# Optimization experiments

Hardware: AMD Instinct MI355X
Metric: run time of the kernel (lower is better)

The kernel has to match this reference:

```python
import jax, jax.numpy as jnp
import numpy as np

N, S, D_IN, D_OUT = 8192, 3, 32, 32


def setup_inputs() -> dict:
    key = jax.random.key(0)
    k1, k2, k3, k4 = jax.random.split(key, 4)
    x = jax.random.normal(k1, (N, D_IN), dtype=jnp.float32)
    adj = jax.random.normal(k2, (S, N, N), dtype=jnp.float32) * 0.01
    # Linear weights per support (W stored as [in, out]; torch Linear is x @ W.T + b,
    # here we store the already-transposed form so pre = x @ W[s] + b[s]).
    W = jax.random.normal(k3, (S, D_IN, D_OUT), dtype=jnp.float32) * (1.0 / np.sqrt(D_IN))
    b = jax.random.normal(k4, (S, D_OUT), dtype=jnp.float32) * 0.01
    return {"x": x, "adj": adj, "W": W, "b": b}


def reference(x, adj, W, b):
    # dropout p=0.0 -> identity
    # per-support linear: pre[s] = x @ W[s] + b[s]  -> [S, N, D_OUT]
    pre = jnp.einsum('ni,sio->sno', x, W) + b[:, None, :]
    # graph propagation + sum over supports: sum_s adj[s] @ pre[s] -> [N, D_OUT]
    out = jnp.einsum('smn,sno->mo', adj, pre)
    return jax.nn.relu(out)
```

## Files before the change

kernel.cpp:

```cpp
#include <hip/hip_runtime.h>
#include <stdint.h>
#include <stddef.h>

static constexpr int NN = 8192;
static constexpr int DD = 32;
static constexpr int SS = 3;

typedef __attribute__((ext_vector_type(8))) short short8;
typedef __attribute__((ext_vector_type(4))) float floatx4;

__device__ __forceinline__ unsigned short f2bf(float f) {
  unsigned int u = __float_as_uint(f);
  u += 0x7FFFu + ((u >> 16) & 1u);
  return (unsigned short)(u >> 16);
}

extern "C" __global__ void __launch_bounds__(256)
pre_kernel(const float* __restrict__ x, const float* __restrict__ W,
           const float* __restrict__ b, unsigned short* __restrict__ preT) {
  __shared__ float xs[256 * 33];
  __shared__ float Ws[DD * DD];
  __shared__ float bs[DD];
  const int t = threadIdx.x;
  const int s = blockIdx.y;
  const int kbase = blockIdx.x * 256;

  #pragma unroll
  for (int j = 0; j < 32; ++j) {
    int idx = j * 256 + t;
    xs[(idx >> 5) * 33 + (idx & 31)] = x[kbase * DD + idx];
  }
  #pragma unroll
  for (int j = 0; j < 4; ++j) Ws[j * 256 + t] = W[s * DD * DD + j * 256 + t];
  if (t < DD) bs[t] = b[s * DD + t];
  __syncthreads();

  float xr[32];
  #pragma unroll
  for (int i = 0; i < 32; ++i) xr[i] = xs[t * 33 + i];

  unsigned short* o = preT + (size_t)s * DD * NN + kbase + t;
  #pragma unroll
  for (int n = 0; n < DD; ++n) {
    float acc = bs[n];
    #pragma unroll
    for (int i = 0; i < 32; ++i) acc += xr[i] * Ws[i * DD + n];
    o[(size_t)n * NN] = f2bf(acc);
  }
}

extern "C" __global__ void __launch_bounds__(512)
prop_kernel(const float* __restrict__ adj, const unsigned short* __restrict__ preT,
            float* __restrict__ out) {
  const int tid  = threadIdx.x;
  const int wave = tid >> 6;
  const int lane = tid & 63;
  const int q = lane >> 4;
  const int c = lane & 15;
  const int m0 = blockIdx.x * 16;

  const float* abase = adj + (size_t)(m0 + c) * NN + q * 8;
  const unsigned short* bbase = preT + (size_t)c * NN + q * 8;

  floatx4 acc0 = {0.f, 0.f, 0.f, 0.f};
  floatx4 acc1 = {0.f, 0.f, 0.f, 0.f};

  #pragma unroll 2
  for (int it = 0; it < 96; ++it) {
    const int st = wave + (it << 3);
    const int s  = st >> 8;
    const int k0 = (st & 255) << 5;

    const float* ap = abase + (size_t)s * NN * NN + k0;
    floatx4 alo = *(const floatx4*)ap;
    floatx4 ahi = *(const floatx4*)(ap + 4);

    const unsigned short* bp = bbase + (size_t)s * DD * NN + k0;
    short8 b0 = *(const short8*)bp;
    short8 b1 = *(const short8*)(bp + (size_t)16 * NN);

    short8 a;
    a[0] = (short)f2bf(alo[0]); a[1] = (short)f2bf(alo[1]);
    a[2] = (short)f2bf(alo[2]); a[3] = (short)f2bf(alo[3]);
    a[4] = (short)f2bf(ahi[0]); a[5] = (short)f2bf(ahi[1]);
    a[6] = (short)f2bf(ahi[2]); a[7] = (short)f2bf(ahi[3]);

    acc0 = __builtin_amdgcn_mfma_f32_16x16x32_bf16(a, b0, acc0, 0, 0, 0);
    acc1 = __builtin_amdgcn_mfma_f32_16x16x32_bf16(a, b1, acc1, 0, 0, 0);
  }

  __shared__ float red[8 * 512];
  #pragma unroll
  for (int r = 0; r < 4; ++r) {
    red[wave * 512 + (q * 4 + r) * 32 + c]      = acc0[r];
    red[wave * 512 + (q * 4 + r) * 32 + 16 + c] = acc1[r];
  }
  __syncthreads();

  float v = 0.f;
  #pragma unroll
  for (int w = 0; w < 8; ++w) v += red[w * 512 + tid];
  v = fmaxf(v, 0.f);
  out[(size_t)m0 * DD + tid] = v;
}

extern "C" void kernel_launch(void* const* d_in, const int* in_sizes, int n_in,
                              void* d_out, int out_size, void* d_ws, size_t ws_size,
                              hipStream_t stream) {
  const float* x   = (const float*)d_in[0];
  const float* adj = (const float*)d_in[1];
  const float* W   = (const float*)d_in[2];
  const float* b   = (const float*)d_in[3];
  float* out = (float*)d_out;
  unsigned short* preT = (unsigned short*)d_ws;

  dim3 g1(NN / 256, SS);
  pre_kernel<<<g1, 256, 0, stream>>>(x, W, b, preT);
  prop_kernel<<<NN / 16, 512, 0, stream>>>(adj, preT, out);
}
```

Measured before the change: 1.041 ms.

## Stage adj tiles through double-buffered LDS with coalesced row loads and register prefetch

The propagation kernel now loads adj with each thread reading 8 contiguous floats of a 256-wide row chunk, so global reads are coalesced. It converts them to bf16 and writes them into a double-buffered LDS tile that waves then read in MFMA fragment layout. Next-chunk global loads are issued before the current chunk is processed. A custom barrier waits only on LDS traffic so outstanding global loads stay in flight, and launch bounds request higher occupancy. The trade-off is one barrier per chunk and extra LDS traffic for a kernel that is limited by memory bandwidth.

```diff
diff --git a/kernel.cpp b/kernel.cpp
--- a/kernel.cpp
+++ b/kernel.cpp
@@ -2,9 +2,13 @@
 #include <stdint.h>
 #include <stddef.h>
 
+
 static constexpr int NN = 8192;
 static constexpr int DD = 32;
 static constexpr int SS = 3;
+static constexpr int KB = 256;
+static constexpr int LSTR = KB + 8;
+static constexpr int NCH = SS * NN / KB;
 
 typedef __attribute__((ext_vector_type(8))) short short8;
 typedef __attribute__((ext_vector_type(4))) float floatx4;
@@ -13,6 +17,10 @@
   unsigned int u = __float_as_uint(f);
   u += 0x7FFFu + ((u >> 16) & 1u);
   return (unsigned short)(u >> 16);
+}
+
+__device__ __forceinline__ void barrier_no_vm_drain() {
+  asm volatile("s_waitcnt lgkmcnt(0)\n\ts_barrier" ::: "memory");
 }
 
 extern "C" __global__ void __launch_bounds__(256)
@@ -49,7 +57,7 @@
   }
 }
 
-extern "C" __global__ void __launch_bounds__(512)
+extern "C" __global__ void __launch_bounds__(512, 4)
 prop_kernel(const float* __restrict__ adj, const unsigned short* __restrict__ preT,
             float* __restrict__ out) {
   const int tid  = threadIdx.x;
@@ -59,37 +67,67 @@
   const int c = lane & 15;
   const int m0 = blockIdx.x * 16;
 
-  const float* abase = adj + (size_t)(m0 + c) * NN + q * 8;
-  const unsigned short* bbase = preT + (size_t)c * NN + q * 8;
+  __shared__ unsigned short As[2][16 * LSTR];
+  __shared__ float red[8 * 512];
+
+  const int srow  = tid >> 5;
+  const int skoff = (tid & 31) * 8;
+  const float* gA = adj + (size_t)(m0 + srow) * NN + skoff;
+
+  const unsigned short* gB = preT + (size_t)c * NN + wave * 32 + q * 8;
 
   floatx4 acc0 = {0.f, 0.f, 0.f, 0.f};
   floatx4 acc1 = {0.f, 0.f, 0.f, 0.f};
 
-  #pragma unroll 2
-  for (int it = 0; it < 96; ++it) {
-    const int st = wave + (it << 3);
-    const int s  = st >> 8;
-    const int k0 = (st & 255) << 5;
+  auto a_addr = [&](int ch) -> const float* {
+    return gA + ((size_t)(ch >> 5) << 26) + ((ch & 31) << 8);
+  };
+  auto b_addr = [&](int ch) -> const unsigned short* {
+    return gB + ((size_t)(ch >> 5) << 18) + ((ch & 31) << 8);
+  };
 
-    const float* ap = abase + (size_t)s * NN * NN + k0;
-    floatx4 alo = *(const floatx4*)ap;
-    floatx4 ahi = *(const floatx4*)(ap + 4);
-
-    const unsigned short* bp = bbase + (size_t)s * DD * NN + k0;
-    short8 b0 = *(const short8*)bp;
-    short8 b1 = *(const short8*)(bp + (size_t)16 * NN);
-
-    short8 a;
-    a[0] = (short)f2bf(alo[0]); a[1] = (short)f2bf(alo[1]);
-    a[2] = (short)f2bf(alo[2]); a[3] = (short)f2bf(alo[3]);
-    a[4] = (short)f2bf(ahi[0]); a[5] = (short)f2bf(ahi[1]);
-    a[6] = (short)f2bf(ahi[2]); a[7] = (short)f2bf(ahi[3]);
-
-    acc0 = __builtin_amdgcn_mfma_f32_16x16x32_bf16(a, b0, acc0, 0, 0, 0);
-    acc1 = __builtin_amdgcn_mfma_f32_16x16x32_bf16(a, b1, acc1, 0, 0, 0);
+  floatx4 ca0, ca1;
+  short8  cb0, cb1;
+  {
+    const float* p = a_addr(0);
+    ca0 = *(const floatx4*)p;
+    ca1 = *(const floatx4*)(p + 4);
+    const unsigned short* bp = b_addr(0);
+    cb0 = *(const short8*)bp;
+    cb1 = *(const short8*)(bp + 16 * NN);
   }
 
-  __shared__ float red[8 * 512];
+  unsigned short* const dst0 = &As[0][srow * LSTR + skoff];
+  unsigned short* const dst1 = &As[1][srow * LSTR + skoff];
+  const unsigned short* const af0 = &As[0][c * LSTR + wave * 32 + q * 8];
+  const unsigned short* const af1 = &As[1][c * LSTR + wave * 32 + q * 8];
+
+  #pragma unroll 2
+  for (int ch = 0; ch < NCH; ++ch) {
+    const int chn = (ch + 1 < NCH) ? ch + 1 : NCH - 1;
+    const float* pa = a_addr(chn);
+    floatx4 na0 = *(const floatx4*)pa;
+    floatx4 na1 = *(const floatx4*)(pa + 4);
+    const unsigned short* pb = b_addr(chn);
+    short8 nb0 = *(const short8*)pb;
+    short8 nb1 = *(const short8*)(pb + 16 * NN);
+
+    short8 w;
+    w[0] = (short)f2bf(ca0[0]); w[1] = (short)f2bf(ca0[1]);
+    w[2] = (short)f2bf(ca0[2]); w[3] = (short)f2bf(ca0[3]);
+    w[4] = (short)f2bf(ca1[0]); w[5] = (short)f2bf(ca1[1]);
+    w[6] = (short)f2bf(ca1[2]); w[7] = (short)f2bf(ca1[3]);
+    *(short8*)((ch & 1) ? dst1 : dst0) = w;
+
+    barrier_no_vm_drain();
+
+    const short8 a = *(const short8*)((ch & 1) ? af1 : af0);
+    acc0 = __builtin_amdgcn_mfma_f32_16x16x32_bf16(a, cb0, acc0, 0, 0, 0);
+    acc1 = __builtin_amdgcn_mfma_f32_16x16x32_bf16(a, cb1, acc1, 0, 0, 0);
+
+    ca0 = na0; ca1 = na1; cb0 = nb0; cb1 = nb1;
+  }
+
   #pragma unroll
   for (int r = 0; r < 4; ++r) {
     red[wave * 512 + (q * 4 + r) * 32 + c]      = acc0[r];
@@ -99,9 +137,8 @@
 
   float v = 0.f;
   #pragma unroll
-  for (int w = 0; w < 8; ++w) v += red[w * 512 + tid];
-  v = fmaxf(v, 0.f);
-  out[(size_t)m0 * DD + tid] = v;
+  for (int w2 = 0; w2 < 8; ++w2) v += red[w2 * 512 + tid];
+  out[(size_t)m0 * DD + tid] = fmaxf(v, 0.f);
 }
 
 extern "C" void kernel_launch(void* const* d_in, const int* in_sizes, int n_in,
```

Measured after the change: 1.015 ms. 1.03x faster.
